# Optimization experiments

Measured on AMD Instinct MI355X. Metric: run time of the kernel, lower is better.

## Reference

```python
import jax, jax.numpy as jnp
import numpy as np

BS, SL, NC = 1024, 512, 50


def setup_inputs() -> dict:
    key = jax.random.key(0)
    k1, k2, k3, k4 = jax.random.split(key, 4)
    inputs = jax.random.normal(k1, (BS, SL, NC), dtype=jnp.float32)
    # variable sentence lengths; mask is True on PAD positions (as in torch code)
    lengths = jax.random.randint(k2, (BS,), SL // 4, SL + 1)
    masks = jnp.arange(SL)[None, :] >= lengths[:, None]
    tag_indices = jax.random.randint(k3, (BS, SL), 0, NC)
    transitions = jax.random.normal(k4, (NC, NC), dtype=jnp.float32) * 0.1
    return {"inputs": inputs, "transitions": transitions,
            "masks": masks, "tag_indices": tag_indices}


def _crf_loss(inputs, transitions, masks, tag_indices):
    bs, sl, nc = inputs.shape
    # unary score: emission of the gold tag at each valid position
    unary = jnp.take_along_axis(inputs, tag_indices[..., None], axis=2)[..., 0]  # [bs,sl]
    unary = jnp.where(masks, 0.0, unary).sum(axis=1)
    # binary score: transition gold[t] -> gold[t+1] where t+1 valid
    binary = transitions[tag_indices[:, :-1], tag_indices[:, 1:]]  # [bs,sl-1]
    binary = jnp.where(masks[:, 1:], 0.0, binary).sum(axis=1)
    # log partition via forward algorithm (fused scan over time)
    alphas0 = inputs[:, 0, :]  # [bs,nc]
    rest_x = jnp.swapaxes(inputs[:, 1:, :], 0, 1)  # [sl-1,bs,nc]
    rest_m = jnp.swapaxes(masks[:, 1:], 0, 1)      # [sl-1,bs]

    def step(alphas, xm):
        x, m = xm
        scores = alphas[:, :, None] + transitions[None, :, :]  # [bs,nc_from,nc_to]
        new_alphas = x + jax.scipy.special.logsumexp(scores, axis=1)
        # carry alphas unchanged at padded positions (masked_scatter_ in torch)
        alphas = jnp.where(m[:, None], alphas, new_alphas)
        return alphas, None

    alphas, _ = jax.lax.scan(step, alphas0, (rest_x, rest_m))
    log_norm = jax.scipy.special.logsumexp(alphas, axis=1)  # [bs]
    log_likelihood = unary + binary - log_norm
    loss = -log_likelihood.sum() / bs  # batch_average=True
    return loss


def reference(inputs, transitions, masks, tag_indices):
    loss = _crf_loss(inputs, transitions, masks, tag_indices)
    return loss, transitions
```

## Files before the change

kernel.cpp:

```cpp
#include <hip/hip_runtime.h>


#define BS 1024
#define SL 512
#define NC 50

#define RLF(v, i) __int_as_float(__builtin_amdgcn_readlane(__float_as_int(v), i))
#define RFLF(v)   __int_as_float(__builtin_amdgcn_readfirstlane(__float_as_int(v)))

#define EC(q) make_float4(__expf(T_s[(4*(q)+0)*NC+jj]), __expf(T_s[(4*(q)+1)*NC+jj]), \
                          __expf(T_s[(4*(q)+2)*NC+jj]), __expf(T_s[(4*(q)+3)*NC+jj]))
#define ER(q) make_float4(__expf(T_s[jj*NC+4*(q)+0]), __expf(T_s[jj*NC+4*(q)+1]), \
                          __expf(T_s[jj*NC+4*(q)+2]), __expf(T_s[jj*NC+4*(q)+3]))

#define QUAD(k, E) \
  s0 = fmaf(RLF(Vv, 4*k+0), E.x, s0); \
  s1 = fmaf(RLF(Vv, 4*k+1), E.y, s1); \
  s2 = fmaf(RLF(Vv, 4*k+2), E.z, s2); \
  s3 = fmaf(RLF(Vv, 4*k+3), E.w, s3);

#define DOT50(dst) \
  float s0 = RLF(Vv, 0) * e0.x; \
  float s1 = RLF(Vv, 1) * e0.y; \
  float s2 = RLF(Vv, 2) * e0.z; \
  float s3 = RLF(Vv, 3) * e0.w; \
  QUAD(1, e1)  QUAD(2, e2)  QUAD(3, e3)  QUAD(4, e4)  QUAD(5, e5) \
  QUAD(6, e6)  QUAD(7, e7)  QUAD(8, e8)  QUAD(9, e9)  QUAD(10, e10) QUAD(11, e11) \
  s0 = fmaf(RLF(Vv, 48), e12.x, s0); \
  s1 = fmaf(RLF(Vv, 49), e12.y, s1); \
  const float dst = (s0 + s1) + (s2 + s3);

__launch_bounds__(128, 2)
__global__ void crf_fused(const float* __restrict__ inputs,
                          const float* __restrict__ trans,
                          const int* __restrict__ masks,
                          const int* __restrict__ tags,
                          float* __restrict__ out) {
  __shared__ float T_s[NC * NC];
  __shared__ float Bb_s[64];
  __shared__ float scal[2];

  const int tid = threadIdx.x;
  const int w = tid >> 6;
  const int j = tid & 63;
  const int b = blockIdx.x;
  const bool jv = (j < NC);
  const int jj = jv ? j : (NC - 1);

  for (int k = tid; k < NC * NC; k += 128) T_s[k] = trans[k];
  __syncthreads();

  if (b == 0) {
    for (int k = tid; k < NC * NC; k += 128) out[1 + k] = T_s[k];
  }

  const float* __restrict__ xr = inputs + (size_t)b * SL * NC;
  const int* __restrict__ mr = masks + b * SL;
  const int* __restrict__ gr = tags + b * SL;

  int nm = 0;
#pragma unroll
  for (int c = 0; c < 8; ++c) {
    nm += (int)__popcll(__ballot(mr[c * 64 + j] != 0));
  }
  const int L = SL - nm;
  const int mid = L >> 1;

  float u = 0.0f;
#pragma unroll
  for (int c = 0; c < 4; ++c) {
    const int t = (w * 4 + c) * 64 + j;
    const int g = gr[t];
    const int tp = (t >= 1) ? t - 1 : 0;
    const int gp = gr[tp];
    float add = xr[(size_t)t * NC + g];
    if (t >= 1) add += T_s[gp * NC + g];
    if (t < L) u += add;
  }
#pragma unroll
  for (int m = 32; m; m >>= 1) u += __shfl_xor(u, m, 64);

  if (w == 0) {
    float4 e0 = EC(0), e1 = EC(1), e2 = EC(2),  e3 = EC(3);
    float4 e4 = EC(4), e5 = EC(5), e6 = EC(6),  e7 = EC(7);
    float4 e8 = EC(8), e9 = EC(9), e10 = EC(10), e11 = EC(11);
    float2 e12 = make_float2(__expf(T_s[48 * NC + jj]), __expf(T_s[49 * NC + jj]));

    float Vv = __expf(xr[jj]);
    float C = 0.0f;

    float xc = xr[1 * NC + jj];
    float p1 = xr[2 * NC + jj];
    float p2 = xr[3 * NC + jj];
    float p3 = xr[4 * NC + jj];

    for (int t = 1; t <= mid; ++t) {
      const float ex = __expf(xc);
      const float r = RFLF(Vv);
      DOT50(dot)
      C += __logf(r);
      Vv = (ex * __builtin_amdgcn_rcpf(r)) * dot;
      xc = p1; p1 = p2; p2 = p3;
      p3 = xr[(t + 4) * NC + jj];
    }
    const float rf = RFLF(Vv);
    C += __logf(rf);
    const float A = Vv * __builtin_amdgcn_rcpf(rf);

    __syncthreads();
    float prod = jv ? (A * Bb_s[j]) : 0.0f;
#pragma unroll
    for (int m = 32; m; m >>= 1) prod += __shfl_xor(prod, m, 64);
    if (j == 0) {
      const float logZ = C + scal[0] + __logf(prod);
      const float ll = (u + scal[1]) - logZ;
      atomicAdd(out, -ll * (1.0f / (float)BS));
    }
  } else {
    float4 e0 = ER(0), e1 = ER(1), e2 = ER(2),  e3 = ER(3);
    float4 e4 = ER(4), e5 = ER(5), e6 = ER(6),  e7 = ER(7);
    float4 e8 = ER(8), e9 = ER(9), e10 = ER(10), e11 = ER(11);
    float2 e12 = make_float2(__expf(T_s[jj * NC + 48]), __expf(T_s[jj * NC + 49]));

    float B = 1.0f;
    float Cb = 0.0f;

    float xc = xr[(L - 1) * NC + jj];
    float p1 = xr[(L - 2) * NC + jj];
    float p2 = xr[(L - 3) * NC + jj];
    float p3 = xr[(L - 4) * NC + jj];

    for (int t = L - 1; t > mid; --t) {
      const float ex = __expf(xc);
      const float r = RFLF(B);
      const float Vv = ex * B;
      DOT50(dot)
      Cb += __logf(r);
      B = __builtin_amdgcn_rcpf(r) * dot;
      xc = p1; p1 = p2; p2 = p3;
      p3 = xr[(t - 4) * NC + jj];
    }
    const float rf = RFLF(B);
    Cb += __logf(rf);
    Bb_s[j] = B * __builtin_amdgcn_rcpf(rf);
    if (j == 0) { scal[0] = Cb; scal[1] = u; }
    __syncthreads();
  }
}

extern "C" void kernel_launch(void* const* d_in, const int* in_sizes, int n_in,
                              void* d_out, int out_size, void* d_ws, size_t ws_size,
                              hipStream_t stream) {
  const float* inputs = (const float*)d_in[0];
  const float* trans  = (const float*)d_in[1];
  const int*   masks  = (const int*)d_in[2];
  const int*   tags   = (const int*)d_in[3];
  float* out = (float*)d_out;

  crf_fused<<<BS, 128, 0, stream>>>(inputs, trans, masks, tags, out);
}
```

Baseline: 313.2 us.

## Use packed fp16 dot2 with lane-pair swizzle for the 50-wide recurrence dot

Each step's 50-term dot product now runs in fp16. A ds_swizzle pairs adjacent lanes' alpha values into one packed fp16 word, which cuts the readlane broadcasts from 50 to 25. The 25 v_dot2 instructions use pre-packed exp(transition) pairs instead of 50 fp32 FMAs. An extra scale of e^-2 per step, with +2 added to the log accumulator, keeps the values inside fp16 range. This shortens the serial per-step chain but lowers precision and risks fp16 overflow or underflow on other inputs.

Measured after the change: 287.4 us. 8.2% less time.

```diff
diff --git a/kernel.cpp b/kernel.cpp
--- a/kernel.cpp
+++ b/kernel.cpp
@@ -5,30 +5,58 @@
 #define SL 512
 #define NC 50
 
-#define RLF(v, i) __int_as_float(__builtin_amdgcn_readlane(__float_as_int(v), i))
-#define RFLF(v)   __int_as_float(__builtin_amdgcn_readfirstlane(__float_as_int(v)))
+typedef _Float16 h2 __attribute__((ext_vector_type(2)));
 
-#define EC(q) make_float4(__expf(T_s[(4*(q)+0)*NC+jj]), __expf(T_s[(4*(q)+1)*NC+jj]), \
-                          __expf(T_s[(4*(q)+2)*NC+jj]), __expf(T_s[(4*(q)+3)*NC+jj]))
-#define ER(q) make_float4(__expf(T_s[jj*NC+4*(q)+0]), __expf(T_s[jj*NC+4*(q)+1]), \
-                          __expf(T_s[jj*NC+4*(q)+2]), __expf(T_s[jj*NC+4*(q)+3]))
+#define RFLF(v) __int_as_float(__builtin_amdgcn_readfirstlane(__float_as_int(v)))
 
-#define QUAD(k, E) \
-  s0 = fmaf(RLF(Vv, 4*k+0), E.x, s0); \
-  s1 = fmaf(RLF(Vv, 4*k+1), E.y, s1); \
-  s2 = fmaf(RLF(Vv, 4*k+2), E.z, s2); \
-  s3 = fmaf(RLF(Vv, 4*k+3), E.w, s3);
+#if defined(__has_builtin)
+#if __has_builtin(__builtin_amdgcn_fdot2)
+#define HAVE_FDOT2 1
+#endif
+#endif
+#ifndef HAVE_FDOT2
+#define HAVE_FDOT2 0
+#endif
 
-#define DOT50(dst) \
-  float s0 = RLF(Vv, 0) * e0.x; \
-  float s1 = RLF(Vv, 1) * e0.y; \
-  float s2 = RLF(Vv, 2) * e0.z; \
-  float s3 = RLF(Vv, 3) * e0.w; \
-  QUAD(1, e1)  QUAD(2, e2)  QUAD(3, e3)  QUAD(4, e4)  QUAD(5, e5) \
-  QUAD(6, e6)  QUAD(7, e7)  QUAD(8, e8)  QUAD(9, e9)  QUAD(10, e10) QUAD(11, e11) \
-  s0 = fmaf(RLF(Vv, 48), e12.x, s0); \
-  s1 = fmaf(RLF(Vv, 49), e12.y, s1); \
-  const float dst = (s0 + s1) + (s2 + s3);
+static __device__ __forceinline__ float fd(unsigned pk, int lane, unsigned ew, float acc) {
+  const unsigned aw = (unsigned)__builtin_amdgcn_readlane((int)pk, lane);
+#if HAVE_FDOT2
+  return __builtin_amdgcn_fdot2(__builtin_bit_cast(h2, aw),
+                                __builtin_bit_cast(h2, ew), acc, false);
+#else
+  const h2 A = __builtin_bit_cast(h2, aw);
+  const h2 E = __builtin_bit_cast(h2, ew);
+  return fmaf((float)A.y, (float)E.y, fmaf((float)A.x, (float)E.x, acc));
+#endif
+}
+
+#define PKE(x, y) __builtin_bit_cast(unsigned, __builtin_amdgcn_cvt_pkrtz(__expf(x), __expf(y)))
+
+#define E_DECL unsigned e0,e1,e2,e3,e4,e5,e6,e7,e8,e9,e10,e11,e12,e13,e14,e15, \
+                        e16,e17,e18,e19,e20,e21,e22,e23,e24;
+#define AP25(M) M(0) M(1) M(2) M(3) M(4) M(5) M(6) M(7) M(8) M(9) M(10) M(11) \
+                M(12) M(13) M(14) M(15) M(16) M(17) M(18) M(19) M(20) M(21) M(22) M(23) M(24)
+#define IF(q) e##q = PKE(T_s[(2*(q))*NC + jj], T_s[(2*(q)+1)*NC + jj]);
+#define IB(q) e##q = PKE(T_s[jj*NC + 2*(q)], T_s[jj*NC + 2*(q)+1]);
+
+#define PACK_BCAST(Vb) \
+  const int pr_ = __builtin_amdgcn_ds_swizzle(__float_as_int(Vb), 0x041F); \
+  const unsigned pk = __builtin_bit_cast(unsigned, \
+      __builtin_amdgcn_cvt_pkrtz((Vb), __int_as_float(pr_)));
+
+#define DOT25() \
+  float a0 = fd(pk, 0, e0, 0.f); float a1 = fd(pk, 2, e1, 0.f); \
+  float a2 = fd(pk, 4, e2, 0.f); float a3 = fd(pk, 6, e3, 0.f); \
+  float a4 = fd(pk, 8, e4, 0.f); \
+  a0 = fd(pk,10,e5 ,a0); a1 = fd(pk,12,e6 ,a1); a2 = fd(pk,14,e7 ,a2); \
+  a3 = fd(pk,16,e8 ,a3); a4 = fd(pk,18,e9 ,a4); \
+  a0 = fd(pk,20,e10,a0); a1 = fd(pk,22,e11,a1); a2 = fd(pk,24,e12,a2); \
+  a3 = fd(pk,26,e13,a3); a4 = fd(pk,28,e14,a4); \
+  a0 = fd(pk,30,e15,a0); a1 = fd(pk,32,e16,a1); a2 = fd(pk,34,e17,a2); \
+  a3 = fd(pk,36,e18,a3); a4 = fd(pk,38,e19,a4); \
+  a0 = fd(pk,40,e20,a0); a1 = fd(pk,42,e21,a1); a2 = fd(pk,44,e22,a2); \
+  a3 = fd(pk,46,e23,a3); a4 = fd(pk,48,e24,a4); \
+  const float dot = ((a0 + a1) + (a2 + a3)) + a4;
 
 __launch_bounds__(128, 2)
 __global__ void crf_fused(const float* __restrict__ inputs,
@@ -81,12 +109,10 @@
   for (int m = 32; m; m >>= 1) u += __shfl_xor(u, m, 64);
 
   if (w == 0) {
-    float4 e0 = EC(0), e1 = EC(1), e2 = EC(2),  e3 = EC(3);
-    float4 e4 = EC(4), e5 = EC(5), e6 = EC(6),  e7 = EC(7);
-    float4 e8 = EC(8), e9 = EC(9), e10 = EC(10), e11 = EC(11);
-    float2 e12 = make_float2(__expf(T_s[48 * NC + jj]), __expf(T_s[49 * NC + jj]));
+    E_DECL
+    AP25(IF)
 
-    float Vv = __expf(xr[jj]);
+    float V = __expf(xr[jj]);
     float C = 0.0f;
 
     float xc = xr[1 * NC + jj];
@@ -96,16 +122,17 @@
 
     for (int t = 1; t <= mid; ++t) {
       const float ex = __expf(xc);
-      const float r = RFLF(Vv);
-      DOT50(dot)
-      C += __logf(r);
-      Vv = (ex * __builtin_amdgcn_rcpf(r)) * dot;
+      const float r = RFLF(V);
+      PACK_BCAST(V)
+      DOT25()
+      C += __logf(r) + 2.0f;
+      V = (ex * (__builtin_amdgcn_rcpf(r) * 0.13533528f)) * dot;
       xc = p1; p1 = p2; p2 = p3;
       p3 = xr[(t + 4) * NC + jj];
     }
-    const float rf = RFLF(Vv);
+    const float rf = RFLF(V);
     C += __logf(rf);
-    const float A = Vv * __builtin_amdgcn_rcpf(rf);
+    const float A = V * __builtin_amdgcn_rcpf(rf);
 
     __syncthreads();
     float prod = jv ? (A * Bb_s[j]) : 0.0f;
@@ -117,13 +144,11 @@
       atomicAdd(out, -ll * (1.0f / (float)BS));
     }
   } else {
-    float4 e0 = ER(0), e1 = ER(1), e2 = ER(2),  e3 = ER(3);
-    float4 e4 = ER(4), e5 = ER(5), e6 = ER(6),  e7 = ER(7);
-    float4 e8 = ER(8), e9 = ER(9), e10 = ER(10), e11 = ER(11);
-    float2 e12 = make_float2(__expf(T_s[jj * NC + 48]), __expf(T_s[jj * NC + 49]));
+    E_DECL
+    AP25(IB)
 
-    float B = 1.0f;
-    float Cb = 0.0f;
+    float V = 1.0f;
+    float C = 0.0f;
 
     float xc = xr[(L - 1) * NC + jj];
     float p1 = xr[(L - 2) * NC + jj];
@@ -132,18 +157,19 @@
 
     for (int t = L - 1; t > mid; --t) {
       const float ex = __expf(xc);
-      const float r = RFLF(B);
-      const float Vv = ex * B;
-      DOT50(dot)
-      Cb += __logf(r);
-      B = __builtin_amdgcn_rcpf(r) * dot;
+      const float r = RFLF(V);
+      const float W = ex * V;
+      PACK_BCAST(W)
+      DOT25()
+      C += __logf(r) + 2.0f;
+      V = (__builtin_amdgcn_rcpf(r) * 0.13533528f) * dot;
       xc = p1; p1 = p2; p2 = p3;
       p3 = xr[(t - 4) * NC + jj];
     }
-    const float rf = RFLF(B);
-    Cb += __logf(rf);
-    Bb_s[j] = B * __builtin_amdgcn_rcpf(rf);
-    if (j == 0) { scal[0] = Cb; scal[1] = u; }
+    const float rf = RFLF(V);
+    C += __logf(rf);
+    Bb_s[j] = V * __builtin_amdgcn_rcpf(rf);
+    if (j == 0) { scal[0] = C; scal[1] = u; }
     __syncthreads();
   }
 }
```
